# Optimization experiments

Hardware: AMD Instinct MI355X
Metric: run time of the kernel (lower is better)

The kernel has to match this reference:

```python
import jax, jax.numpy as jnp
import numpy as np

TEMP = 0.05
EPS = 1e-8  # matches torch F.cosine_similarity eps
B, D = 8192, 1024


def setup_inputs() -> dict:
    key = jax.random.key(0)
    k1, k2, k3 = jax.random.split(key, 3)
    return {
        "premise": jax.random.normal(k1, (B, D), dtype=jnp.float32),
        "entail": jax.random.normal(k2, (B, D), dtype=jnp.float32),
        "contra": jax.random.normal(k3, (B, D), dtype=jnp.float32),
    }


def _l2norm(x):
    # F.cosine_similarity clamps norms at eps
    n = jnp.sqrt(jnp.sum(x * x, axis=-1, keepdims=True))
    return x / jnp.maximum(n, EPS)


def reference(premise, entail, contra):
    p = _l2norm(premise)
    e = _l2norm(entail)
    c = _l2norm(contra)
    sim_pre_ent = jnp.einsum("bd,nd->bn", p, e) / TEMP        # [B, B]
    sim_pre_contra = jnp.einsum("bd,nd->bn", p, c) / TEMP     # [B, B]
    sims = jnp.concatenate([sim_pre_ent, sim_pre_contra], axis=-1)  # [B, 2B]
    # cross entropy with label = arange(B): target is the diagonal of the first B columns
    logz = jax.nn.logsumexp(sims, axis=-1)                    # [B]
    tgt = jnp.diagonal(sim_pre_ent)                           # logits[i, i]
    loss = jnp.mean(logz - tgt)
    return (loss, sims)
```

## Files before the change

kernel.cpp:

```cpp
#include <hip/hip_runtime.h>
#include <hip/hip_bf16.h>
#include <cstdint>
#include <cstddef>

#define BDIM 8192
#define DDIM 1024
#define NCOL 16384
#define TEMP_INV 20.0f

typedef __bf16 bf16;
typedef bf16 bf16x4 __attribute__((ext_vector_type(4)));
typedef bf16 bf16x8 __attribute__((ext_vector_type(8)));
typedef float f32x4 __attribute__((ext_vector_type(4)));

__device__ __forceinline__ void load_lds16(const void* g, void* l) {
    __builtin_amdgcn_global_load_lds(
        (const __attribute__((address_space(1))) void*)g,
        (__attribute__((address_space(3))) void*)l, 16, 0, 0);
}

__global__ __launch_bounds__(256) void norm_kernel(
    const float* __restrict__ P, const float* __restrict__ E,
    const float* __restrict__ C,
    bf16* __restrict__ Pb, bf16* __restrict__ Eb, bf16* __restrict__ Cb,
    float* __restrict__ rowsum)
{
    int b = blockIdx.x;
    int which = b >> 13;
    int row = b & (BDIM - 1);
    const float* src = (which == 0) ? P : (which == 1 ? E : C);
    bf16* dst = (which == 0) ? Pb : (which == 1 ? Eb : Cb);
    src += (size_t)row * DDIM;
    dst += (size_t)row * DDIM;

    int t = threadIdx.x;
    if (b < 32) rowsum[b * 256 + t] = 0.0f;

    float4 v = ((const float4*)src)[t];
    float ss = v.x * v.x + v.y * v.y + v.z * v.z + v.w * v.w;
    #pragma unroll
    for (int m = 32; m >= 1; m >>= 1) ss += __shfl_xor(ss, m, 64);

    __shared__ float wsum[4];
    if ((t & 63) == 0) wsum[t >> 6] = ss;
    __syncthreads();
    float tot = wsum[0] + wsum[1] + wsum[2] + wsum[3];
    float inv = 1.0f / fmaxf(sqrtf(tot), 1e-8f);

    bf16x4 o;
    o[0] = (bf16)(v.x * inv);
    o[1] = (bf16)(v.y * inv);
    o[2] = (bf16)(v.z * inv);
    o[3] = (bf16)(v.w * inv);
    ((bf16x4*)dst)[t] = o;
}

__global__ __launch_bounds__(256) void gemm_kernel(
    const bf16* __restrict__ Pb, const bf16* __restrict__ Eb,
    const bf16* __restrict__ Cb,
    float* __restrict__ sims,
    float* __restrict__ rowsum)
{
    const int ct = blockIdx.x;
    const int rt = blockIdx.y;
    const bf16* Bsrc = (ct < 64) ? Eb : Cb;
    const int nb = (ct & 63) * 128;
    const int mb = rt * 128;

    __shared__ bf16 As[128 * 32];
    __shared__ bf16 Bs[128 * 32];

    const int t = threadIdx.x;
    const int lane = t & 63;
    const int wave = t >> 6;
    const int wr = (wave >> 1) * 64;
    const int wc = (wave & 1) * 64;
    const int quad = lane >> 4;
    const int l15 = lane & 15;

    const int srow = t >> 2;
    const int scol = (t & 3) * 8;
    const bf16* ga = Pb   + (size_t)(mb + srow) * DDIM + scol;
    const bf16* gb = Bsrc + (size_t)(nb + srow) * DDIM + scol;
    bf16* la = As + t * 8;
    bf16* lb = Bs + t * 8;

    f32x4 acc[4][4];
    #pragma unroll
    for (int i = 0; i < 4; i++)
        #pragma unroll
        for (int j = 0; j < 4; j++) {
            f32x4 z = {0.f, 0.f, 0.f, 0.f};
            acc[i][j] = z;
        }

    for (int kt = 0; kt < DDIM; kt += 32) {
        __syncthreads();
        load_lds16(ga + kt,                la);
        load_lds16(ga + kt + 64 * DDIM,    la + 64 * 32);
        load_lds16(gb + kt,                lb);
        load_lds16(gb + kt + 64 * DDIM,    lb + 64 * 32);
        __syncthreads();

        bf16x8 af[4], bfr[4];
        #pragma unroll
        for (int i = 0; i < 4; i++)
            af[i] = *(const bf16x8*)(As + (wr + i * 16 + l15) * 32 + quad * 8);
        #pragma unroll
        for (int j = 0; j < 4; j++)
            bfr[j] = *(const bf16x8*)(Bs + (wc + j * 16 + l15) * 32 + quad * 8);

        #pragma unroll
        for (int i = 0; i < 4; i++)
            #pragma unroll
            for (int j = 0; j < 4; j++)
                acc[i][j] = __builtin_amdgcn_mfma_f32_16x16x32_bf16(
                    af[i], bfr[j], acc[i][j], 0, 0, 0);
    }

    const int gcolbase = ct * 128 + wc + l15;
    #pragma unroll
    for (int i = 0; i < 4; i++) {
        #pragma unroll
        for (int r = 0; r < 4; r++) {
            const int grow = mb + wr + i * 16 + quad * 4 + r;
            float* orow = sims + (size_t)grow * NCOL;
            float rs = 0.f;
            #pragma unroll
            for (int j = 0; j < 4; j++) {
                float v = acc[i][j][r] * TEMP_INV;
                orow[gcolbase + j * 16] = v;
                rs += __expf(v);
            }
            rs += __shfl_xor(rs, 1, 64);
            rs += __shfl_xor(rs, 2, 64);
            rs += __shfl_xor(rs, 4, 64);
            rs += __shfl_xor(rs, 8, 64);
            if (l15 == 0) atomicAdd(&rowsum[grow], rs);
        }
    }
}

__global__ __launch_bounds__(1024) void finalize_kernel(
    const float* __restrict__ rowsum, const float* __restrict__ sims,
    float* __restrict__ out)
{
    int t = threadIdx.x;
    float s = 0.f;
    for (int i = t; i < BDIM; i += 1024) {
        float logz = logf(rowsum[i]);
        float tgt = sims[(size_t)i * NCOL + i];
        s += logz - tgt;
    }
    #pragma unroll
    for (int m = 32; m >= 1; m >>= 1) s += __shfl_xor(s, m, 64);
    __shared__ float ws[16];
    if ((t & 63) == 0) ws[t >> 6] = s;
    __syncthreads();
    if (t == 0) {
        float tot = 0.f;
        #pragma unroll
        for (int k = 0; k < 16; k++) tot += ws[k];
        out[0] = tot / (float)BDIM;
    }
}

extern "C" void kernel_launch(void* const* d_in, const int* in_sizes, int n_in,
                              void* d_out, int out_size, void* d_ws, size_t ws_size,
                              hipStream_t stream) {
    const float* P = (const float*)d_in[0];
    const float* E = (const float*)d_in[1];
    const float* C = (const float*)d_in[2];
    float* out = (float*)d_out;
    float* sims = out + 1;

    constexpr size_t MAT_BYTES = (size_t)BDIM * DDIM * sizeof(bf16);
    uint8_t* ws = (uint8_t*)d_ws;
    bf16* Pb = (bf16*)(ws);
    bf16* Eb = (bf16*)(ws + MAT_BYTES);
    bf16* Cb = (bf16*)(ws + 2 * MAT_BYTES);
    float* rowsum = (float*)(ws + 3 * MAT_BYTES);

    norm_kernel<<<3 * BDIM, 256, 0, stream>>>(P, E, C, Pb, Eb, Cb, rowsum);
    dim3 grid(128, 64);
    gemm_kernel<<<grid, 256, 0, stream>>>(Pb, Eb, Cb, sims, rowsum);
    finalize_kernel<<<1, 1024, 0, stream>>>(rowsum, sims, out);
}
```

Before: 995.6 us.

## Restructure GEMM into 256x256 tiles with double-buffered swizzled LDS pipeline

Replaces the 128x128 single-buffered GEMM, which synchronises twice per K-step, with a 256x256-tile, 512-thread kernel. It double-buffers 64-wide K slabs in 128KB of LDS, XOR-swizzles the LDS layout to avoid bank conflicts, and interleaves global-to-LDS staging with MFMA phases using barriers, waitcnt and s_setprio. It also remaps block IDs for L2 locality and switches the sims writes to nontemporal stores. The aim is to raise MFMA utilisation and hide memory latency. The cost is high register use (8x4 accumulators) and fragile hand scheduling with inline asm.

```diff
diff --git a/kernel.cpp b/kernel.cpp
--- a/kernel.cpp
+++ b/kernel.cpp
@@ -7,16 +7,28 @@
 #define DDIM 1024
 #define NCOL 16384
 #define TEMP_INV 20.0f
+#define NT 16
 
 typedef __bf16 bf16;
 typedef bf16 bf16x4 __attribute__((ext_vector_type(4)));
 typedef bf16 bf16x8 __attribute__((ext_vector_type(8)));
 typedef float f32x4 __attribute__((ext_vector_type(4)));
+typedef int   i32x4 __attribute__((ext_vector_type(4)));
 
 __device__ __forceinline__ void load_lds16(const void* g, void* l) {
     __builtin_amdgcn_global_load_lds(
         (const __attribute__((address_space(1))) void*)g,
         (__attribute__((address_space(3))) void*)l, 16, 0, 0);
+}
+
+__device__ __forceinline__ bf16x8 ds_read128(unsigned off) {
+    i32x4 r;
+    asm volatile("ds_read_b128 %0, %1" : "=v"(r) : "v"(off));
+    return __builtin_bit_cast(bf16x8, r);
+}
+
+__device__ __forceinline__ unsigned lds_off(const void* p) {
+    return (unsigned)(unsigned long long)(const __attribute__((address_space(3))) void*)p;
 }
 
 __global__ __launch_bounds__(256) void norm_kernel(
@@ -55,81 +67,158 @@
     ((bf16x4*)dst)[t] = o;
 }
 
-__global__ __launch_bounds__(256) void gemm_kernel(
+#define MIDBAR() do { __builtin_amdgcn_s_barrier(); \
+    asm volatile("s_waitcnt lgkmcnt(0)" ::: "memory"); \
+    __builtin_amdgcn_sched_barrier(0); \
+    __builtin_amdgcn_s_setprio(1); } while (0)
+#define ENDP() do { __builtin_amdgcn_s_setprio(0); \
+    __builtin_amdgcn_s_barrier(); } while (0)
+#define ENDPV(N) do { __builtin_amdgcn_s_setprio(0); \
+    asm volatile("s_waitcnt vmcnt(" #N ")" ::: "memory"); \
+    __builtin_amdgcn_s_barrier(); } while (0)
+
+__global__ __launch_bounds__(512, 2) void gemm_kernel(
     const bf16* __restrict__ Pb, const bf16* __restrict__ Eb,
     const bf16* __restrict__ Cb,
     float* __restrict__ sims,
     float* __restrict__ rowsum)
 {
-    const int ct = blockIdx.x;
-    const int rt = blockIdx.y;
-    const bf16* Bsrc = (ct < 64) ? Eb : Cb;
-    const int nb = (ct & 63) * 128;
-    const int mb = rt * 128;
-
-    __shared__ bf16 As[128 * 32];
-    __shared__ bf16 Bs[128 * 32];
-
-    const int t = threadIdx.x;
+    __shared__ __align__(16) char smem[131072];
+
+    const int bid = blockIdx.x;
+    const int sid = (bid & 7) * 256 + (bid >> 3);
+    const int ct = sid & 63;
+    const int rt = sid >> 6;
+
+    const char* Asrc = (const char*)Pb + (size_t)rt * 256 * 2048;
+    const char* Bsrc = (const char*)((ct < 32) ? Eb : Cb)
+                     + (size_t)(ct & 31) * 256 * 2048;
+
+    const int t    = threadIdx.x;
     const int lane = t & 63;
     const int wave = t >> 6;
-    const int wr = (wave >> 1) * 64;
-    const int wc = (wave & 1) * 64;
-    const int quad = lane >> 4;
-    const int l15 = lane & 15;
-
-    const int srow = t >> 2;
-    const int scol = (t & 3) * 8;
-    const bf16* ga = Pb   + (size_t)(mb + srow) * DDIM + scol;
-    const bf16* gb = Bsrc + (size_t)(nb + srow) * DDIM + scol;
-    bf16* la = As + t * 8;
-    bf16* lb = Bs + t * 8;
-
-    f32x4 acc[4][4];
-    #pragma unroll
-    for (int i = 0; i < 4; i++)
+    const int wm   = wave >> 2;
+    const int wn   = wave & 3;
+    const int q    = lane >> 4;
+    const int l15  = lane & 15;
+    const int c7   = l15 & 7;
+
+    const char* gAp[2]; const char* gBp[2];
+    #pragma unroll
+    for (int u = 0; u < 2; u++) {
+        int L = u * 8192 + t * 16;
+        int T = L ^ (((L >> 7) & 7) << 4);
+        gAp[u] = Asrc + (size_t)(T >> 7) * 2048 + (T & 127);
+        gBp[u] = Bsrc + (size_t)(T >> 7) * 2048 + (T & 127);
+    }
+
+    const unsigned LB    = lds_off(smem);
+    const unsigned baseA = LB + (unsigned)(wm * 16384 + l15 * 128);
+    const unsigned baseB = LB + 65536u
+                         + (unsigned)((wn >> 1) * 16384 + ((wn & 1) * 64 + l15) * 128);
+    const unsigned ck0   = (unsigned)((q ^ c7) << 4);
+
+    char* const ldst = smem + t * 16;
+    auto stageA = [&](int buf, int half, int kt) {
+        char* l = ldst + buf * 32768 + half * 16384;
+        const char* g0 = gAp[0] + (size_t)half * 262144 + (size_t)kt * 128;
+        const char* g1 = gAp[1] + (size_t)half * 262144 + (size_t)kt * 128;
+        load_lds16(g0, l);
+        load_lds16(g1, l + 8192);
+    };
+    auto stageB = [&](int buf, int half, int kt) {
+        char* l = ldst + 65536 + buf * 32768 + half * 16384;
+        const char* g0 = gBp[0] + (size_t)half * 262144 + (size_t)kt * 128;
+        const char* g1 = gBp[1] + (size_t)half * 262144 + (size_t)kt * 128;
+        load_lds16(g0, l);
+        load_lds16(g1, l + 8192);
+    };
+
+    f32x4 acc[8][4];
+    #pragma unroll
+    for (int i = 0; i < 8; i++)
         #pragma unroll
         for (int j = 0; j < 4; j++) {
             f32x4 z = {0.f, 0.f, 0.f, 0.f};
             acc[i][j] = z;
         }
 
-    for (int kt = 0; kt < DDIM; kt += 32) {
-        __syncthreads();
-        load_lds16(ga + kt,                la);
-        load_lds16(ga + kt + 64 * DDIM,    la + 64 * 32);
-        load_lds16(gb + kt,                lb);
-        load_lds16(gb + kt + 64 * DDIM,    lb + 64 * 32);
-        __syncthreads();
-
-        bf16x8 af[4], bfr[4];
-        #pragma unroll
-        for (int i = 0; i < 4; i++)
-            af[i] = *(const bf16x8*)(As + (wr + i * 16 + l15) * 32 + quad * 8);
-        #pragma unroll
-        for (int j = 0; j < 4; j++)
-            bfr[j] = *(const bf16x8*)(Bs + (wc + j * 16 + l15) * 32 + quad * 8);
-
-        #pragma unroll
-        for (int i = 0; i < 4; i++)
-            #pragma unroll
-            for (int j = 0; j < 4; j++)
-                acc[i][j] = __builtin_amdgcn_mfma_f32_16x16x32_bf16(
-                    af[i], bfr[j], acc[i][j], 0, 0, 0);
-    }
-
-    const int gcolbase = ct * 128 + wc + l15;
-    #pragma unroll
-    for (int i = 0; i < 4; i++) {
+    bf16x8 af[4][2], bfr[2][2], bg[2][2];
+
+    auto rdA = [&](bf16x8 (&d)[4][2], int buf, int ib) {
+        unsigned base = baseA + (unsigned)buf * 32768u + (unsigned)ib * 2048u;
+        #pragma unroll
+        for (int ii = 0; ii < 4; ii++)
+            #pragma unroll
+            for (int kk = 0; kk < 2; kk++)
+                d[ii][kk] = ds_read128(base + (unsigned)ii * 2048u + (ck0 ^ (kk << 6)));
+    };
+    auto rdB = [&](bf16x8 (&d)[2][2], int buf, int jb) {
+        unsigned base = baseB + (unsigned)buf * 32768u + (unsigned)jb * 2048u;
+        #pragma unroll
+        for (int jj = 0; jj < 2; jj++)
+            #pragma unroll
+            for (int kk = 0; kk < 2; kk++)
+                d[jj][kk] = ds_read128(base + (unsigned)jj * 2048u + (ck0 ^ (kk << 6)));
+    };
+    auto mm16 = [&](int ib, int jb, bf16x8 (&A)[4][2], bf16x8 (&Bv)[2][2]) {
+        #pragma unroll
+        for (int ii = 0; ii < 4; ii++)
+            #pragma unroll
+            for (int jj = 0; jj < 2; jj++)
+                #pragma unroll
+                for (int kk = 0; kk < 2; kk++)
+                    acc[ib + ii][jb + jj] = __builtin_amdgcn_mfma_f32_16x16x32_bf16(
+                        A[ii][kk], Bv[jj][kk], acc[ib + ii][jb + jj], 0, 0, 0);
+    };
+
+    stageA(0, 0, 0); stageA(0, 1, 0); stageB(0, 0, 0); stageB(0, 1, 0);
+    stageA(1, 0, 1);
+    asm volatile("s_waitcnt vmcnt(2)" ::: "memory");
+    __builtin_amdgcn_s_barrier();
+
+    for (int m = 0; m < NT / 2; ++m) {
+        const int k1 = 2 * m + 1, k2 = 2 * m + 2, k3 = 2 * m + 3;
+        const bool st = (m < NT / 2 - 1);
+        rdA(af, 0, 0); rdB(bfr, 0, 0);
+        stageA(1, 1, k1);
+        MIDBAR(); mm16(0, 0, af, bfr); ENDP();
+        rdB(bg, 0, 2);
+        stageB(1, 0, k1);
+        MIDBAR(); mm16(0, 2, af, bg); ENDP();
+        rdA(af, 0, 4);
+        stageB(1, 1, k1);
+        MIDBAR(); mm16(4, 2, af, bg); ENDP();
+        if (st) stageA(0, 0, k2);
+        MIDBAR(); mm16(4, 0, af, bfr);
+        if (st) { ENDPV(2); } else { ENDPV(0); }
+        rdA(af, 1, 0); rdB(bfr, 1, 0);
+        if (st) stageA(0, 1, k2);
+        MIDBAR(); mm16(0, 0, af, bfr); ENDP();
+        rdB(bg, 1, 2);
+        if (st) stageB(0, 0, k2);
+        MIDBAR(); mm16(0, 2, af, bg); ENDP();
+        rdA(af, 1, 4);
+        if (st) stageB(0, 1, k2);
+        MIDBAR(); mm16(4, 2, af, bg); ENDP();
+        if (st) stageA(1, 0, k3);
+        MIDBAR(); mm16(4, 0, af, bfr);
+        ENDPV(2);
+    }
+
+    const int gr0 = rt * 256 + wm * 128 + q * 4;
+    const int gc0 = ct * 256 + wn * 64 + l15;
+    #pragma unroll
+    for (int i = 0; i < 8; i++) {
         #pragma unroll
         for (int r = 0; r < 4; r++) {
-            const int grow = mb + wr + i * 16 + quad * 4 + r;
+            const int grow = gr0 + i * 16 + r;
             float* orow = sims + (size_t)grow * NCOL;
             float rs = 0.f;
             #pragma unroll
             for (int j = 0; j < 4; j++) {
                 float v = acc[i][j][r] * TEMP_INV;
-                orow[gcolbase + j * 16] = v;
+                __builtin_nontemporal_store(v, orow + gc0 + j * 16);
                 rs += __expf(v);
             }
             rs += __shfl_xor(rs, 1, 64);
@@ -182,7 +271,6 @@
     float* rowsum = (float*)(ws + 3 * MAT_BYTES);
 
     norm_kernel<<<3 * BDIM, 256, 0, stream>>>(P, E, C, Pb, Eb, Cb, rowsum);
-    dim3 grid(128, 64);
-    gemm_kernel<<<grid, 256, 0, stream>>>(Pb, Eb, Cb, sims, rowsum);
+    gemm_kernel<<<2048, 512, 0, stream>>>(Pb, Eb, Cb, sims, rowsum);
     finalize_kernel<<<1, 1024, 0, stream>>>(rowsum, sims, out);
 }
```

Result: faster. 963.0 us (-3.3%).
